# Kernel tuning notes

Hardware: AMD Instinct MI355X
Metric: run time of the kernel (lower is better)

## Reference

```python
import jax, jax.numpy as jnp
import numpy as np

NUM_HEADS = 16
GRID_SIZE = 16


def rotate(x, pos):
    # x: [B, nH, N, D] with D even; pos: [N] float
    D = x.shape[-1]
    half = D // 2
    omega = jnp.arange(half, dtype=x.dtype) / half
    omega = 1.0 / (10000.0 ** omega)
    freq = pos[:, None].astype(x.dtype) * omega          # [N, half]
    # torch .repeat(1,1,1,2) TILES the last dim (not interleave)
    emb_sin = jnp.tile(jnp.sin(freq), (1, 2))            # [N, D]
    emb_cos = jnp.tile(jnp.cos(freq), (1, 2))
    y = x.reshape(x.shape[:-1] + (half, 2))
    rot = jnp.stack((-y[..., 1], y[..., 0]), axis=-1).reshape(x.shape)
    return x * emb_cos + rot * emb_sin


def setup_inputs() -> dict:
    key = jax.random.key(0)
    k1, k2, k3, k4 = jax.random.split(key, 4)
    B, N, C = 2, 2048, 1024
    return {
        "x": jax.random.normal(k1, (B, N, C), dtype=jnp.float32),
        "W_qkv": jax.random.normal(k2, (3 * C, C), dtype=jnp.float32) * 0.02,
        "W_proj": jax.random.normal(k3, (C, C), dtype=jnp.float32) * 0.02,
        "b_proj": jax.random.normal(k4, (C,), dtype=jnp.float32) * 0.02,
        "T": 8,
        "H": 16,
        "W": 16,
    }


def reference(x, W_qkv, W_proj, b_proj, T, H, W):
    B, N, C = x.shape
    nH = NUM_HEADS
    hd = C // nH
    d_dim = 2 * (hd // 3 // 2)   # 20 for hd=64
    h_dim = d_dim
    w_dim = d_dim

    # axial positions (mask=None path): ids = arange(T*H*W)
    ids = jnp.arange(T * H * W)
    d_pos = (ids // (H * W)).astype(jnp.float32)
    rem = ids % (H * W)
    h_pos = (rem // W).astype(jnp.float32) * (GRID_SIZE / H)
    w_pos = (rem % W).astype(jnp.float32) * (GRID_SIZE / W)

    # fused QKV projection (no bias)
    qkv = jnp.einsum('bnc,oc->bno', x, W_qkv)            # [B, N, 3C]
    qkv = qkv.reshape(B, N, 3, nH, hd).transpose(2, 0, 3, 1, 4)
    q, k, v = qkv[0], qkv[1], qkv[2]                     # [B, nH, N, hd]

    s0, s1, s2 = 0, d_dim, d_dim + h_dim
    s3 = s2 + w_dim
    qd = rotate(q[..., s0:s1], d_pos); kd = rotate(k[..., s0:s1], d_pos)
    qh = rotate(q[..., s1:s2], h_pos); kh = rotate(k[..., s1:s2], h_pos)
    qw = rotate(q[..., s2:s3], w_pos); kw = rotate(k[..., s2:s3], w_pos)
    if s3 < hd:
        q = jnp.concatenate([qd, qh, qw, q[..., s3:]], axis=-1)
        k = jnp.concatenate([kd, kh, kw, k[..., s3:]], axis=-1)
    else:
        q = jnp.concatenate([qd, qh, qw], axis=-1)
        k = jnp.concatenate([kd, kh, kw], axis=-1)

    # SDPA (default scale = hd**-0.5, no dropout, not causal)
    scale = hd ** (-0.5)
    scores = jnp.einsum('bhqd,bhkd->bhqk', q, k) * scale
    attn = jax.nn.softmax(scores, axis=-1)
    out = jnp.einsum('bhqk,bhkd->bhqd', attn, v)          # [B, nH, N, hd]

    out = out.transpose(0, 2, 1, 3).reshape(B, N, C)
    out = jnp.einsum('bnc,oc->bno', out, W_proj) + b_proj
    return out


if __name__ == "__main__":
    inp = setup_inputs()
    y = reference(**inp)
    print(y.shape, y.dtype)
```

## Files before the change

### kernel.cpp

```cpp
#include <hip/hip_runtime.h>
#include <stdint.h>

typedef unsigned short u16;
typedef __attribute__((ext_vector_type(8))) short bf16x8;
typedef __attribute__((ext_vector_type(4))) float f32x4;
typedef __attribute__((ext_vector_type(16))) float f32x16;
typedef __attribute__((ext_vector_type(2))) unsigned int u32x2;

#define DEVI static __device__ __forceinline__

static constexpr int NTOK = 2048;
static constexpr int CDIM = 1024;
static constexpr int C3   = 3072;

DEVI u16 f2bf(float f) {
  uint32_t u = __float_as_uint(f);
  return (u16)((u + 0x7fffu + ((u >> 16) & 1u)) >> 16);
}

DEVI float exp2fast(float x) { return __builtin_amdgcn_exp2f(x); }

DEVI void gl_lds16(const void* g, void* l) {
  __builtin_amdgcn_global_load_lds(
      (__attribute__((address_space(1))) uint32_t*)g,
      (__attribute__((address_space(3))) uint32_t*)l, 16, 0, 0);
}

DEVI f32x4 mfma16(bf16x8 a, bf16x8 b, f32x4 c) {
  return __builtin_amdgcn_mfma_f32_16x16x32_bf16(a, b, c, 0, 0, 0);
}
DEVI f32x16 mfma32(bf16x8 a, bf16x8 b, f32x16 c) {
  return __builtin_amdgcn_mfma_f32_32x32x16_bf16(a, b, c, 0, 0, 0);
}

__global__ void k_cvt3(const float* __restrict__ x, const float* __restrict__ wq,
                       const float* __restrict__ wp, u16* __restrict__ xb,
                       u16* __restrict__ wqb, u16* __restrict__ wpb) {
  int i = (blockIdx.x * blockDim.x + threadIdx.x) * 4;
  const float* src; u16* dst; int off;
  if (i < 4194304)      { src = x;  dst = xb;  off = i; }
  else if (i < 7340032) { src = wq; dst = wqb; off = i - 4194304; }
  else                  { src = wp; dst = wpb; off = i - 7340032; }
  float4 v = *reinterpret_cast<const float4*>(src + off);
  ushort4 o;
  o.x = f2bf(v.x); o.y = f2bf(v.y); o.z = f2bf(v.z); o.w = f2bf(v.w);
  *reinterpret_cast<ushort4*>(dst + off) = o;
}

template<int MODE>
__global__ __launch_bounds__(256, 2) void k_gemm(
    const u16* __restrict__ A, const u16* __restrict__ Bw,
    float* __restrict__ Cout, const float* __restrict__ bias,
    u16* __restrict__ qb, u16* __restrict__ kb, u16* __restrict__ vT,
    int Nn, int K) {
  constexpr int NJ = (MODE == 1) ? 2 : 4;
  constexpr int WN = NJ * 16;
  __shared__ u16 smem[MODE == 2 ? 17408 : 6144];
  u16* Al = smem;
  u16* Bl = smem + 4096;
  const int tid = threadIdx.x, wid = tid >> 6, lane = tid & 63;
  const int bm = blockIdx.x, bn = blockIdx.y;
  const int wr = wid >> 1, wc = wid & 1;
  const int fr = lane & 15, fg = lane >> 4;
  f32x4 acc[4][NJ] = {};

  const int r0 = wid * 16 + (lane >> 2);
  const int c0 = (lane & 3) * 8;
  const u16* Ag = A + (size_t)(bm * 128) * K + c0;
  const u16* Bg = Bw + (size_t)(bn * (MODE == 1 ? 64 : 128)) * K + c0;
  u16* Alb = Al + wid * 512;
  u16* Blb = Bl + wid * 512;
  const int fk = fg * 8;

  for (int kt = 0; kt < K; kt += 32) {
    __syncthreads();
    gl_lds16(Ag + (size_t)r0 * K + kt,        Alb);
    gl_lds16(Ag + (size_t)(64 + r0) * K + kt, Alb + 2048);
    gl_lds16(Bg + (size_t)r0 * K + kt,        Blb);
    if constexpr (MODE == 2)
      gl_lds16(Bg + (size_t)(64 + r0) * K + kt, Blb + 2048);
    __syncthreads();
    bf16x8 af[4], bfr[NJ];
#pragma unroll
    for (int i = 0; i < 4; ++i)
      af[i] = *reinterpret_cast<const bf16x8*>(&Al[(wr * 64 + i * 16 + fr) * 32 + fk]);
#pragma unroll
    for (int j = 0; j < NJ; ++j)
      bfr[j] = *reinterpret_cast<const bf16x8*>(&Bl[(wc * WN + j * 16 + fr) * 32 + fk]);
#pragma unroll
    for (int i = 0; i < 4; ++i)
#pragma unroll
      for (int j = 0; j < NJ; ++j)
        acc[i][j] = mfma16(af[i], bfr[j], acc[i][j]);
  }
  const int orow0 = bm * 128 + wr * 64 + fg * 4;

  if constexpr (MODE == 1) {
    const int ocol0 = bn * 64 + wc * 32 + fr;
#pragma unroll
    for (int j = 0; j < NJ; ++j) {
      int col = ocol0 + j * 16;
      float badd = bias[col];
#pragma unroll
      for (int i = 0; i < 4; ++i)
#pragma unroll
        for (int r = 0; r < 4; ++r)
          Cout[(size_t)(orow0 + i * 16 + r) * Nn + col] = acc[i][j][r] + badd;
    }
  } else {
    const int which = bn >> 3;
    if (which < 2) {
      const int cbase = (bn & 7) * 128 + wc * 64 + fr;
      u16* dst = (which == 0) ? qb : kb;
#pragma unroll
      for (int j = 0; j < 4; ++j) {
        const int c = cbase + j * 16;
        const int d = c & 63, hh = c >> 6;
        const bool dorope = (d < 60);
        int seg = 0; float omega = 0.f;
        if (dorope) {
          seg = d / 20;
          int ds = d - seg * 20;
          int jj = (ds >= 10) ? ds - 10 : ds;
          omega = exp2fast(-1.3287712379549449f * (float)jj);
        }
#pragma unroll
        for (int i = 0; i < 4; ++i) {
#pragma unroll
          for (int r = 0; r < 4; ++r) {
            const int m = orow0 + i * 16 + r;
            const int b = m >> 11, n = m & (NTOK - 1);
            float val = acc[i][j][r];
            float pr = __shfl_xor(val, 1, 64);
            float outv = val;
            if (dorope) {
              float pos = (seg == 0) ? (float)(n >> 8)
                        : (seg == 1) ? (float)((n >> 4) & 15)
                                     : (float)(n & 15);
              float f = pos * omega, sn, cs;
              __sincosf(f, &sn, &cs);
              outv = (d & 1) ? val * cs + pr * sn : val * cs - pr * sn;
            }
            if (which == 0) outv *= 0.18033688011112042f;
            dst[((size_t)(b * 16 + hh) * NTOK + n) * 64 + d] = f2bf(outv);
          }
        }
      }
    } else {
      __syncthreads();
      const int mbase = wr * 64 + fg * 4;
#pragma unroll
      for (int j = 0; j < 4; ++j) {
        const int crow = wc * 64 + j * 16 + fr;
#pragma unroll
        for (int i = 0; i < 4; ++i) {
          ushort4 pk;
          pk.x = f2bf(acc[i][j][0]); pk.y = f2bf(acc[i][j][1]);
          pk.z = f2bf(acc[i][j][2]); pk.w = f2bf(acc[i][j][3]);
          *reinterpret_cast<ushort4*>(&smem[crow * 136 + mbase + i * 16]) = pk;
        }
      }
      __syncthreads();
      const int c = tid >> 1, mh = (tid & 1) * 64;
      const int cfull = (bn & 7) * 128 + c;
      const int hh = cfull >> 6, d = cfull & 63;
      const int b = bm >> 4;
      u16* dst = vT + (((size_t)(b * 16 + hh)) * 64 + d) * NTOK + (bm & 15) * 128 + mh;
      const u16* srcl = &smem[c * 136 + mh];
#pragma unroll
      for (int s = 0; s < 8; ++s)
        *reinterpret_cast<bf16x8*>(dst + s * 8) = *reinterpret_cast<const bf16x8*>(srcl + s * 8);
    }
  }
}

__global__ __launch_bounds__(256, 1) void k_attn(
    const u16* __restrict__ qp, const u16* __restrict__ kp,
    const u16* __restrict__ vp, u16* __restrict__ op) {
  __shared__ u16 Kl[2][64 * 64];
  __shared__ u16 Vl[2][64 * 64];
  const int bh = blockIdx.x;
  const int qt = blockIdx.y;
  const int tid = threadIdx.x, wid = tid >> 6, lane = tid & 63;
  const int lo = lane & 31, hi = lane >> 5;

  int koff[4];
#pragma unroll
  for (int c = 0; c < 4; ++c) koff[c] = (((c * 2 + hi) ^ (lo & 7)) * 8);
  const int lbase = lo * 64;

  const int q0 = qt * 256 + wid * 64;
  bf16x8 qf[2][4];
#pragma unroll
  for (int qa = 0; qa < 2; ++qa) {
    const u16* qrow = qp + ((size_t)bh * NTOK + q0 + qa * 32 + lo) * 64 + hi * 8;
#pragma unroll
    for (int c = 0; c < 4; ++c)
      qf[qa][c] = *reinterpret_cast<const bf16x8*>(qrow + c * 16);
  }

  f32x16 acc2[2][2] = {};
  float lrun[2] = {0.f, 0.f};

  const int srow = lane >> 3;
  const int scol = ((lane & 7) ^ srow) * 8;
  const u16* kg = kp + ((size_t)bh * NTOK + wid * 8 + srow) * 64 + scol;
  const u16* vg = vp + ((size_t)bh * 64 + wid * 8 + srow) * NTOK + scol;

  auto stage = [&](int buf, int kvt) {
#pragma unroll
    for (int s = 0; s < 2; ++s) {
      gl_lds16(kg + (size_t)(kvt + s * 32) * 64, &Kl[buf][s * 2048 + wid * 512]);
      gl_lds16(vg + (size_t)(s * 32) * NTOK + kvt, &Vl[buf][s * 2048 + wid * 512]);
    }
  };

  stage(0, 0);
  __syncthreads();
  int cur = 0;
  for (int kvt = 0; kvt < NTOK; kvt += 64) {
    if (kvt + 64 < NTOK) stage(cur ^ 1, kvt + 64);
    const u16* Kc = &Kl[cur][0];
    const u16* Vc = &Vl[cur][0];
    float ps[2] = {0.f, 0.f};

#pragma unroll
    for (int mt = 0; mt < 2; ++mt) {
      const u16* Kh = Kc + mt * 2048 + lbase;
      bf16x8 kf[4];
#pragma unroll
      for (int c = 0; c < 4; ++c)
        kf[c] = *reinterpret_cast<const bf16x8*>(Kh + koff[c]);

      bf16x8 pa[2][2];
#pragma unroll
      for (int qa = 0; qa < 2; ++qa) {
        f32x16 s = {};
        __builtin_amdgcn_s_setprio(1);
#pragma unroll
        for (int c = 0; c < 4; ++c) s = mfma32(kf[c], qf[qa][c], s);
        __builtin_amdgcn_s_setprio(0);

        uint32_t pk[8];
#pragma unroll
        for (int jj = 0; jj < 8; ++jj) {
          float p0 = exp2fast(s[2 * jj]);
          float p1 = exp2fast(s[2 * jj + 1]);
          ps[qa] += p0 + p1;
          uint32_t w;
          asm("v_cvt_pk_bf16_f32 %0, %1, %2" : "=v"(w) : "v"(p0), "v"(p1));
          pk[jj] = w;
        }
#pragma unroll
        for (int ksl = 0; ksl < 2; ++ksl) {
          const int g = ksl * 4;
          u32x2 sA = __builtin_amdgcn_permlane32_swap(pk[g + 0], pk[g + 2], false, false);
          u32x2 sB = __builtin_amdgcn_permlane32_swap(pk[g + 1], pk[g + 3], false, false);
          union { uint32_t u[4]; bf16x8 v; } x;
          x.u[0] = sA[0]; x.u[1] = sB[0]; x.u[2] = sA[1]; x.u[3] = sB[1];
          pa[qa][ksl] = x.v;
        }
      }

      __builtin_amdgcn_s_setprio(1);
#pragma unroll
      for (int nf = 0; nf < 2; ++nf) {
        const u16* Vh = Vc + nf * 2048 + lbase;
#pragma unroll
        for (int ksl = 0; ksl < 2; ++ksl) {
          bf16x8 vf = *reinterpret_cast<const bf16x8*>(Vh + koff[mt * 2 + ksl]);
          acc2[0][nf] = mfma32(pa[0][ksl], vf, acc2[0][nf]);
          acc2[1][nf] = mfma32(pa[1][ksl], vf, acc2[1][nf]);
        }
      }
      __builtin_amdgcn_s_setprio(0);
    }

#pragma unroll
    for (int qa = 0; qa < 2; ++qa) {
      float p = ps[qa];
      p += __shfl_xor(p, 32, 64);
      lrun[qa] += p;
    }
    __syncthreads();
    cur ^= 1;
  }

  const int b = bh >> 4, h = bh & 15;
#pragma unroll
  for (int qa = 0; qa < 2; ++qa) {
    float linv[16];
#pragma unroll
    for (int r = 0; r < 16; ++r)
      linv[r] = 1.f / __shfl(lrun[qa], (r & 3) + 8 * (r >> 2) + 4 * hi, 64);
#pragma unroll
    for (int nf = 0; nf < 2; ++nf)
#pragma unroll
      for (int r = 0; r < 16; ++r) {
        int n = q0 + qa * 32 + (r & 3) + 8 * (r >> 2) + 4 * hi;
        int col = h * 64 + nf * 32 + lo;
        op[((size_t)b * NTOK + n) * CDIM + col] = f2bf(acc2[qa][nf][r] * linv[r]);
      }
  }
}

extern "C" void kernel_launch(void* const* d_in, const int* in_sizes, int n_in,
                              void* d_out, int out_size, void* d_ws, size_t ws_size,
                              hipStream_t stream) {
  (void)in_sizes; (void)n_in; (void)out_size; (void)ws_size;
  const float* x  = (const float*)d_in[0];
  const float* Wq = (const float*)d_in[1];
  const float* Wp = (const float*)d_in[2];
  const float* bp = (const float*)d_in[3];

  char* w = (char*)d_ws;
  u16* x_bf  = (u16*)(w + 0);
  u16* wq_bf = (u16*)(w + 8388608);
  u16* wp_bf = (u16*)(w + 14680064);
  u16* q_bf  = (u16*)(w + 16777216);
  u16* k_bf  = (u16*)(w + 25165824);
  u16* vT    = (u16*)(w + 33554432);
  u16* at_bf = (u16*)(w + 41943040);

  k_cvt3<<<8192, 256, 0, stream>>>(x, Wq, Wp, x_bf, wq_bf, wp_bf);

  k_gemm<2><<<dim3(32, 24), 256, 0, stream>>>(x_bf, wq_bf, nullptr, nullptr,
                                              q_bf, k_bf, vT, C3, CDIM);

  k_attn<<<dim3(32, 8), 256, 0, stream>>>(q_bf, k_bf, vT, at_bf);

  k_gemm<1><<<dim3(32, 16), 256, 0, stream>>>(at_bf, wp_bf, (float*)d_out, bp,
                                              nullptr, nullptr, nullptr, CDIM, CDIM);
}
```

Measured before the change: 128.1 us.

## Split attention KV range across two blocks and merge partial results

Adds split-KV parallelism: each attention block now processes half of the key/value sequence (grid z=2), writing unnormalized fp32 partial outputs and row sums to workspace. A new merge kernel adds the two partials, normalizes, and writes bf16 attention output. The goal is to double the attention grid from 256 blocks so the 256 CUs are better occupied, at the cost of extra fp32 global traffic (~32MB written and read) plus an additional launch. The merge relies on the softmax having no running max subtraction, which the kernel already assumes.

```diff
diff --git a/kernel.cpp b/kernel.cpp
--- a/kernel.cpp
+++ b/kernel.cpp
@@ -176,13 +176,16 @@
 
 __global__ __launch_bounds__(256, 1) void k_attn(
     const u16* __restrict__ qp, const u16* __restrict__ kp,
-    const u16* __restrict__ vp, u16* __restrict__ op) {
+    const u16* __restrict__ vp, float* __restrict__ pout,
+    float* __restrict__ plsum) {
   __shared__ u16 Kl[2][64 * 64];
   __shared__ u16 Vl[2][64 * 64];
   const int bh = blockIdx.x;
   const int qt = blockIdx.y;
+  const int z  = blockIdx.z;
   const int tid = threadIdx.x, wid = tid >> 6, lane = tid & 63;
   const int lo = lane & 31, hi = lane >> 5;
+  const int kvbase = z << 10;
 
   int koff[4];
 #pragma unroll
@@ -215,11 +218,11 @@
     }
   };
 
-  stage(0, 0);
+  stage(0, kvbase);
   __syncthreads();
   int cur = 0;
-  for (int kvt = 0; kvt < NTOK; kvt += 64) {
-    if (kvt + 64 < NTOK) stage(cur ^ 1, kvt + 64);
+  for (int kvt = kvbase; kvt < kvbase + 1024; kvt += 64) {
+    if (kvt + 64 < kvbase + 1024) stage(cur ^ 1, kvt + 64);
     const u16* Kc = &Kl[cur][0];
     const u16* Vc = &Vl[cur][0];
     float ps[2] = {0.f, 0.f};
@@ -286,22 +289,38 @@
     cur ^= 1;
   }
 
-  const int b = bh >> 4, h = bh & 15;
+  const size_t pbase = ((size_t)(z * 32 + bh)) * (NTOK * 64);
 #pragma unroll
   for (int qa = 0; qa < 2; ++qa) {
-    float linv[16];
-#pragma unroll
-    for (int r = 0; r < 16; ++r)
-      linv[r] = 1.f / __shfl(lrun[qa], (r & 3) + 8 * (r >> 2) + 4 * hi, 64);
 #pragma unroll
     for (int nf = 0; nf < 2; ++nf)
 #pragma unroll
       for (int r = 0; r < 16; ++r) {
         int n = q0 + qa * 32 + (r & 3) + 8 * (r >> 2) + 4 * hi;
-        int col = h * 64 + nf * 32 + lo;
-        op[((size_t)b * NTOK + n) * CDIM + col] = f2bf(acc2[qa][nf][r] * linv[r]);
-      }
-  }
+        pout[pbase + (size_t)n * 64 + nf * 32 + lo] = acc2[qa][nf][r];
+      }
+    if (hi == 0)
+      plsum[(size_t)(z * 32 + bh) * NTOK + q0 + qa * 32 + lo] = lrun[qa];
+  }
+}
+
+__global__ void k_merge(const float* __restrict__ pout, const float* __restrict__ plsum,
+                        u16* __restrict__ ob) {
+  int t = blockIdx.x * blockDim.x + threadIdx.x;
+  int base = t * 4;
+  int b = base >> 21, n = (base >> 10) & (NTOK - 1), c = base & (CDIM - 1);
+  int bh = b * 16 + (c >> 6), d = c & 63;
+  const size_t zstride = (size_t)32 * NTOK * 64;
+  size_t pidx = (size_t)bh * (NTOK * 64) + (size_t)n * 64 + d;
+  float4 p0 = *reinterpret_cast<const float4*>(pout + pidx);
+  float4 p1 = *reinterpret_cast<const float4*>(pout + zstride + pidx);
+  float rinv = 1.f / (plsum[(size_t)bh * NTOK + n] + plsum[(size_t)(32 + bh) * NTOK + n]);
+  ushort4 o;
+  o.x = f2bf((p0.x + p1.x) * rinv);
+  o.y = f2bf((p0.y + p1.y) * rinv);
+  o.z = f2bf((p0.z + p1.z) * rinv);
+  o.w = f2bf((p0.w + p1.w) * rinv);
+  *reinterpret_cast<ushort4*>(ob + base) = o;
 }
 
 extern "C" void kernel_launch(void* const* d_in, const int* in_sizes, int n_in,
@@ -314,20 +333,23 @@
   const float* bp = (const float*)d_in[3];
 
   char* w = (char*)d_ws;
-  u16* x_bf  = (u16*)(w + 0);
-  u16* wq_bf = (u16*)(w + 8388608);
-  u16* wp_bf = (u16*)(w + 14680064);
-  u16* q_bf  = (u16*)(w + 16777216);
-  u16* k_bf  = (u16*)(w + 25165824);
-  u16* vT    = (u16*)(w + 33554432);
-  u16* at_bf = (u16*)(w + 41943040);
+  u16*   x_bf  = (u16*)  (w + 0);
+  u16*   wq_bf = (u16*)  (w + 8388608);
+  u16*   wp_bf = (u16*)  (w + 14680064);
+  u16*   q_bf  = (u16*)  (w + 16777216);
+  u16*   k_bf  = (u16*)  (w + 25165824);
+  u16*   vT    = (u16*)  (w + 33554432);
+  u16*   at_bf = (u16*)  (w + 41943040);
+  float* pout  = (float*)(w + 50331648);
+  float* plsum = (float*)(w + 83886080);
 
   k_cvt3<<<8192, 256, 0, stream>>>(x, Wq, Wp, x_bf, wq_bf, wp_bf);
 
   k_gemm<2><<<dim3(32, 24), 256, 0, stream>>>(x_bf, wq_bf, nullptr, nullptr,
                                               q_bf, k_bf, vT, C3, CDIM);
 
-  k_attn<<<dim3(32, 8), 256, 0, stream>>>(q_bf, k_bf, vT, at_bf);
+  k_attn<<<dim3(32, 8, 2), 256, 0, stream>>>(q_bf, k_bf, vT, pout, plsum);
+  k_merge<<<4096, 256, 0, stream>>>(pout, plsum, at_bf);
 
   k_gemm<1><<<dim3(32, 16), 256, 0, stream>>>(at_bf, wp_bf, (float*)d_out, bp,
                                               nullptr, nullptr, nullptr, CDIM, CDIM);
```

Result: no change. 127.5 us (-0.5%).
